# Kernel optimization log

Hardware: AMD Instinct MI355X
Metric: run time of the kernel (lower is better)

Reference implementation:

```python
import jax, jax.numpy as jnp
import numpy as np

N_VIS, N_ASSOC, N_MOTOR, IN_DIM, T = 8192, 4096, 1024, 4096, 16
TAU_MEM, V_TH, TAU_ELIG = 20.0, 1.0, 500.0


def setup_inputs() -> dict:
    key = jax.random.key(0)
    ks = jax.random.split(key, 8)
    visual_input = jax.random.uniform(ks[0], (T, IN_DIM), dtype=jnp.float32)
    noise = jax.random.uniform(ks[1], (T, N_VIS), dtype=jnp.float32)  # replaces torch.rand_like
    dopamine = jax.random.normal(ks[2], (T,), dtype=jnp.float32)
    # visual_encoder: nn.Linear(4096, n_visual) default init (kaiming-uniform-ish); use small uniform
    lim = 1.0 / np.sqrt(IN_DIM)
    W_enc = jax.random.uniform(ks[3], (N_VIS, IN_DIM), minval=-lim, maxval=lim, dtype=jnp.float32)
    b_enc = jax.random.uniform(ks[4], (N_VIS,), minval=-lim, maxval=lim, dtype=jnp.float32)
    # v_to_a / a_to_m: uniform_(0.01, 0.05), no bias
    W_va = jax.random.uniform(ks[5], (N_ASSOC, N_VIS), minval=0.01, maxval=0.05, dtype=jnp.float32)
    W_am = jax.random.uniform(ks[6], (N_MOTOR, N_ASSOC), minval=0.01, maxval=0.05, dtype=jnp.float32)
    return {"visual_input": visual_input, "noise": noise, "dopamine": dopamine,
            "W_enc": W_enc, "b_enc": b_enc, "W_va": W_va, "W_am": W_am}


def reference(visual_input, noise, dopamine, W_enc, b_enc, W_va, W_am):
    decay_m = 1.0 - 1.0 / TAU_MEM
    decay_e = 1.0 - 1.0 / TAU_ELIG
    f32 = jnp.float32

    def step(carry, xs):
        vV, vA, vM, eVA, eAM, Wva, Wam = carry
        x, u, d = xs
        # visual encoding + Bernoulli spikes
        rates = jax.nn.sigmoid(x @ W_enc.T + b_enc)             # [n_visual]
        in_spk = (u < rates * 0.3).astype(f32)
        # LIF: visual layer
        vV = vV * decay_m + in_spk
        v_spk = (vV > V_TH).astype(f32)
        vV = vV * (1.0 - v_spk)
        # LIF: assoc layer
        vA = vA * decay_m + (v_spk @ Wva.T) * 0.1
        a_spk = (vA > V_TH).astype(f32)
        vA = vA * (1.0 - a_spk)
        # LIF: motor layer
        vM = vM * decay_m + (a_spk @ Wam.T) * 0.1
        m_spk = (vM > V_TH).astype(f32)
        vM = vM * (1.0 - m_spk)
        # DA-STDP eligibility traces (rank-1 updates)
        eVA = eVA * decay_e + jnp.outer(v_spk, a_spk) * 0.01    # [n_visual, n_assoc]
        eAM = eAM * decay_e + jnp.outer(a_spk, m_spk) * 0.01    # [n_assoc, n_motor]
        # conditional dopamine-gated weight update
        gate = jnp.abs(d) > 0.1
        Wva_new = jnp.clip(Wva + jnp.clip(d * eVA.T * 0.1, -0.01, 0.01), 0.0, 1.0)
        Wam_new = jnp.clip(Wam + jnp.clip(d * eAM.T * 0.1, -0.01, 0.01), 0.0, 1.0)
        Wva = jnp.where(gate, Wva_new, Wva)
        Wam = jnp.where(gate, Wam_new, Wam)
        eVA = jnp.where(gate, eVA * 0.5, eVA)
        eAM = jnp.where(gate, eAM * 0.5, eAM)
        return (vV, vA, vM, eVA, eAM, Wva, Wam), m_spk

    init = (jnp.zeros(N_VIS, f32), jnp.zeros(N_ASSOC, f32), jnp.zeros(N_MOTOR, f32),
            jnp.zeros((N_VIS, N_ASSOC), f32), jnp.zeros((N_ASSOC, N_MOTOR), f32),
            W_va, W_am)
    _, motor_spikes = jax.lax.scan(step, init, (visual_input, noise, dopamine))
    return motor_spikes  # [T, n_motor]
```

## Files before the change

### kernel.cpp

```cpp
#include <hip/hip_runtime.h>
#include <cstdint>

#define N_VIS   8192
#define N_ASSOC 4096
#define N_MOTOR 1024
#define IN_DIM  4096
#define T_STEPS 16

typedef float f32x4 __attribute__((ext_vector_type(4)));

__device__ __forceinline__ float4 nt_load4(const float4* p) {
    f32x4 r = __builtin_nontemporal_load((const f32x4*)p);
    return make_float4(r.x, r.y, r.z, r.w);
}

template<int COLS, int CS>
__global__ __launch_bounds__(512, 4) void mv_rowwave_kernel(
        const float* __restrict__ Wg, const float* __restrict__ Vg,
        float* __restrict__ Sp, int nrows) {
    constexpr int F4PR = COLS / 4;
    constexpr int SEG4 = F4PR / CS;
    constexpr int NIT  = SEG4 / 64;
    __shared__ float4 vs[2][16 * 64];
    const int tid  = threadIdx.x;
    const int lane = tid & 63, wv = tid >> 6;
    const int rb   = blockIdx.x / CS;
    const int sp   = blockIdx.x % CS;
    const int j0   = rb * 16 + wv * 2;
    const float4* W4a = (const float4*)Wg + (size_t)j0 * F4PR + (size_t)sp * SEG4;
    const float4* W4b = W4a + F4PR;
    const float4* V4  = (const float4*)Vg + (size_t)sp * SEG4;

    float acc[2][T_STEPS];
#pragma unroll
    for (int t = 0; t < T_STEPS; ++t) { acc[0][t] = 0.f; acc[1][t] = 0.f; }

    {
        int f = tid;
#pragma unroll
        for (int p = 0; p < 2; ++p, f += 512) {
            int t = f >> 6, c = f & 63;
            vs[0][f] = V4[(size_t)t * F4PR + c];
        }
    }
    float4 wa = nt_load4(&W4a[lane]), wb = nt_load4(&W4b[lane]);
    __syncthreads();

    int buf = 0;
#pragma unroll 1
    for (int it = 0; it < NIT; ++it) {
        float4 wan = wa, wbn = wb;
        if (it + 1 < NIT) {
            wan = nt_load4(&W4a[(it + 1) * 64 + lane]);
            wbn = nt_load4(&W4b[(it + 1) * 64 + lane]);
            int f = tid;
#pragma unroll
            for (int p = 0; p < 2; ++p, f += 512) {
                int t = f >> 6, c = f & 63;
                vs[buf ^ 1][f] = V4[(size_t)t * F4PR + (it + 1) * 64 + c];
            }
        }
#pragma unroll
        for (int t = 0; t < T_STEPS; ++t) {
            float4 v = vs[buf][t * 64 + lane];
            acc[0][t] = fmaf(wa.x, v.x, acc[0][t]);
            acc[0][t] = fmaf(wa.y, v.y, acc[0][t]);
            acc[0][t] = fmaf(wa.z, v.z, acc[0][t]);
            acc[0][t] = fmaf(wa.w, v.w, acc[0][t]);
            acc[1][t] = fmaf(wb.x, v.x, acc[1][t]);
            acc[1][t] = fmaf(wb.y, v.y, acc[1][t]);
            acc[1][t] = fmaf(wb.z, v.z, acc[1][t]);
            acc[1][t] = fmaf(wb.w, v.w, acc[1][t]);
        }
        __syncthreads();
        wa = wan; wb = wbn; buf ^= 1;
    }

#pragma unroll
    for (int t = 0; t < T_STEPS; ++t) {
        float a0 = acc[0][t], a1 = acc[1][t];
        for (int o = 32; o; o >>= 1) {
            a0 += __shfl_down(a0, o, 64);
            a1 += __shfl_down(a1, o, 64);
        }
        acc[0][t] = a0; acc[1][t] = a1;
    }
    if (lane == 0) {
#pragma unroll
        for (int r = 0; r < 2; ++r) {
            float4* So = (float4*)(Sp + ((size_t)sp * nrows + j0 + r) * 16);
#pragma unroll
            for (int q = 0; q < 4; ++q)
                So[q] = make_float4(acc[r][q*4], acc[r][q*4+1], acc[r][q*4+2], acc[r][q*4+3]);
        }
    }
}

template<int COLS, int CS>
__global__ __launch_bounds__(512, 4) void mv_bits_kernel(
        const float* __restrict__ Wg, const unsigned* __restrict__ mask,
        float* __restrict__ Sp, int nrows) {
    constexpr int F4PR = COLS / 4;
    constexpr int SEG4 = F4PR / CS;
    constexpr int NIT  = SEG4 / 64;
    const int lane = threadIdx.x & 63, wv = threadIdx.x >> 6;
    const int rb   = blockIdx.x / CS;
    const int sp   = blockIdx.x % CS;
    const int j0   = rb * 16 + wv * 2;
    const float4* W4a = (const float4*)Wg + (size_t)j0 * F4PR + (size_t)sp * SEG4;
    const float4* W4b = W4a + F4PR;
    const uint4*  M4  = (const uint4*)mask + (size_t)sp * SEG4;

    float acc0[T_STEPS], acc1[T_STEPS];
#pragma unroll
    for (int t = 0; t < T_STEPS; ++t) { acc0[t] = 0.f; acc1[t] = 0.f; }

#pragma unroll 2
    for (int it = 0; it < NIT; ++it) {
        const int idx = it * 64 + lane;
        float4 wa = nt_load4(&W4a[idx]);
        float4 wb = nt_load4(&W4b[idx]);
        uint4  m  = M4[idx];
#pragma unroll
        for (int t = 0; t < T_STEPS; ++t) {
            float bx = (float)((m.x >> t) & 1u);
            float by = (float)((m.y >> t) & 1u);
            float bz = (float)((m.z >> t) & 1u);
            float bw = (float)((m.w >> t) & 1u);
            acc0[t] = fmaf(wa.x, bx, acc0[t]);
            acc0[t] = fmaf(wa.y, by, acc0[t]);
            acc0[t] = fmaf(wa.z, bz, acc0[t]);
            acc0[t] = fmaf(wa.w, bw, acc0[t]);
            acc1[t] = fmaf(wb.x, bx, acc1[t]);
            acc1[t] = fmaf(wb.y, by, acc1[t]);
            acc1[t] = fmaf(wb.z, bz, acc1[t]);
            acc1[t] = fmaf(wb.w, bw, acc1[t]);
        }
    }

#pragma unroll
    for (int t = 0; t < T_STEPS; ++t) {
        float a0 = acc0[t], a1 = acc1[t];
        for (int o = 32; o; o >>= 1) {
            a0 += __shfl_down(a0, o, 64);
            a1 += __shfl_down(a1, o, 64);
        }
        acc0[t] = a0; acc1[t] = a1;
    }
    if (lane == 0) {
        float4* So0 = (float4*)(Sp + ((size_t)sp * nrows + j0) * 16);
        float4* So1 = (float4*)(Sp + ((size_t)sp * nrows + j0 + 1) * 16);
#pragma unroll
        for (int q = 0; q < 4; ++q) {
            So0[q] = make_float4(acc0[q*4], acc0[q*4+1], acc0[q*4+2], acc0[q*4+3]);
            So1[q] = make_float4(acc1[q*4], acc1[q*4+1], acc1[q*4+2], acc1[q*4+3]);
        }
    }
}

__global__ __launch_bounds__(256) void vlif_kernel(
        const float* __restrict__ S1p, const float* __restrict__ noise,
        const float* __restrict__ b, unsigned* __restrict__ vmask) {
    const int i = blockIdx.x * 256 + threadIdx.x;
    float a[T_STEPS];
#pragma unroll
    for (int t = 0; t < T_STEPS; ++t)
        a[t] = S1p[(size_t)i * 16 + t] + S1p[((size_t)N_VIS + i) * 16 + t];
    const float bb = b[i];
    float v = 0.f;
    unsigned msk = 0;
#pragma unroll
    for (int t = 0; t < T_STEPS; ++t) {
        float logit = a[t] + bb;
        float rate = 1.0f / (1.0f + expf(-logit));
        float u = noise[t * N_VIS + i];
        float ins = (u < rate * 0.3f) ? 1.0f : 0.0f;
        v = v * 0.95f + ins;
        if (v > 1.0f) { msk |= (1u << t); v = 0.f; }
    }
    vmask[i] = msk;
}

__global__ void ktab_kernel(const float* __restrict__ dop, float* __restrict__ K,
                            int* __restrict__ ovl_z) {
    __shared__ float C[256];
    __shared__ float sd[16];
    __shared__ unsigned sg[16];
    const int p = threadIdx.x;
    ovl_z[p] = 0; ovl_z[p + 256] = 0;
    if (p < 16) {
        float d = dop[p];
        sd[p] = d;
        sg[p] = (fabsf(d) > 0.1f) ? 1u : 0u;
    }
    __syncthreads();
    {
        const int s = p >> 4, r = p & 15;
        float c = 0.f;
        if (s >= r) {
            c = 1.f;
            for (int u = r; u < s; ++u) {
                if (sg[u]) c *= 0.5f;
                c *= 0.998f;
            }
        }
        C[p] = c;
    }
    __syncthreads();
    {
        const int t = p >> 4, r = p & 15;
        float kk = 0.f;
        for (int s = r; s < t; ++s)
            if (sg[s]) kk += ((sd[s] * 0.1f) * 0.01f) * C[s * 16 + r];
        K[p] = kk;
    }
}

__global__ void ovl_kernel(const unsigned* __restrict__ mask, int words_per_block,
                           int* __restrict__ ovl) {
    const int p = threadIdx.x;
    const int r = p >> 4, t = p & 15;
    const unsigned* w = mask + blockIdx.x * words_per_block;
    int c = 0;
    for (int i = 0; i < words_per_block; ++i)
        c += (int)((w[i] >> r) & (w[i] >> t) & 1u);
    atomicAdd(&ovl[p], c);
}

__global__ __launch_bounds__(64) void rec_kernel(
        const float* __restrict__ base, const int* __restrict__ ovl,
        const float* __restrict__ K, unsigned* __restrict__ mask_out,
        float* __restrict__ outp, int out_stride, int n_rows, int cs) {
    __shared__ float KO[256];
    const int tid = threadIdx.x;
    for (int p = tid; p < 256; p += 64) {
        const int t = p >> 4, r = p & 15;
        KO[p] = K[p] * (float)ovl[r * 16 + t];
    }
    __syncthreads();

    const int j = blockIdx.x * 64 + tid;
    float br[T_STEPS];
#pragma unroll
    for (int t = 0; t < T_STEPS; ++t) br[t] = base[(size_t)j * 16 + t];
#pragma unroll 1
    for (int s = 1; s < cs; ++s)
#pragma unroll
        for (int t = 0; t < T_STEPS; ++t)
            br[t] += base[((size_t)s * n_rows + j) * 16 + t];

    float vmem = 0.f;
    unsigned am = 0;
#pragma unroll
    for (int t = 0; t < T_STEPS; ++t) {
        float I = br[t];
        for (int r = 0; r < t; ++r)
            if ((am >> r) & 1u) I += KO[t * 16 + r];
        vmem = vmem * 0.95f + I * 0.1f;
        const bool s = vmem > 1.0f;
        if (s) { vmem = 0.f; am |= (1u << t); }
        if (outp) outp[t * out_stride + j] = s ? 1.0f : 0.0f;
    }
    mask_out[j] = am;
}

extern "C" void kernel_launch(void* const* d_in, const int* in_sizes, int n_in,
                              void* d_out, int out_size, void* d_ws, size_t ws_size,
                              hipStream_t stream) {
    const float* x     = (const float*)d_in[0];
    const float* noise = (const float*)d_in[1];
    const float* dop   = (const float*)d_in[2];
    const float* W_enc = (const float*)d_in[3];
    const float* b_enc = (const float*)d_in[4];
    const float* W_va  = (const float*)d_in[5];
    const float* W_am  = (const float*)d_in[6];
    float* out = (float*)d_out;
    (void)in_sizes; (void)n_in; (void)out_size; (void)ws_size;

    char* ws = (char*)d_ws;
    size_t off = 0;
    unsigned* vmask = (unsigned*)(ws + off); off += N_VIS * 4;
    unsigned* amask = (unsigned*)(ws + off); off += N_ASSOC * 4;
    unsigned* mmask = (unsigned*)(ws + off); off += N_MOTOR * 4;
    float*    K     = (float*)(ws + off);    off += 256 * 4;
    int*      ovl_v = (int*)(ws + off);      off += 256 * 4;
    int*      ovl_a = (int*)(ws + off);      off += 256 * 4;
    float*    S1    = (float*)(ws + off);    off += (size_t)2 * N_VIS   * 16 * 4;
    float*    S2    = (float*)(ws + off);    off += (size_t)4 * N_ASSOC * 16 * 4;
    float*    S3    = (float*)(ws + off);    off += (size_t)4 * N_MOTOR * 16 * 4;

    ktab_kernel<<<1, 256, 0, stream>>>(dop, K, ovl_v);
    mv_rowwave_kernel<IN_DIM, 2><<<(N_VIS / 16) * 2, 512, 0, stream>>>(W_enc, x, S1, N_VIS);
    vlif_kernel<<<N_VIS / 256, 256, 0, stream>>>(S1, noise, b_enc, vmask);
    ovl_kernel<<<32, 256, 0, stream>>>(vmask, N_VIS / 32, ovl_v);
    mv_bits_kernel<N_VIS, 4><<<(N_ASSOC / 16) * 4, 512, 0, stream>>>(W_va, vmask, S2, N_ASSOC);
    rec_kernel<<<N_ASSOC / 64, 64, 0, stream>>>(S2, ovl_v, K, amask, nullptr, 0, N_ASSOC, 4);
    ovl_kernel<<<16, 256, 0, stream>>>(amask, N_ASSOC / 16, ovl_a);
    mv_bits_kernel<N_ASSOC, 4><<<(N_MOTOR / 16) * 4, 512, 0, stream>>>(W_am, amask, S3, N_MOTOR);
    rec_kernel<<<N_MOTOR / 64, 64, 0, stream>>>(S3, ovl_a, K, mmask, out, N_MOTOR, N_MOTOR, 4);
}
```

Measured before the change: 146.2 us.

## Fuse matvec, LIF recurrence and overlap counting into per-layer kernels

Each layer's matvec is merged with its LIF/recurrence epilogue and the spike-overlap histogram, and the column split across blocks is dropped so each block owns whole rows. This cuts the launch count from nine to four and removes the partial-sum workspace round trips and the separate ovl kernels. The trade-off is fewer blocks per layer (smaller grids of 256/128 threads for the later layers), longer serial loops per wave, and the serial LIF epilogue running on lane 0 of each wave.

Result: faster. 140.4 us (-3.9%).

```diff
diff --git a/kernel.cpp b/kernel.cpp
--- a/kernel.cpp
+++ b/kernel.cpp
@@ -14,26 +14,59 @@
     return make_float4(r.x, r.y, r.z, r.w);
 }
 
-template<int COLS, int CS>
-__global__ __launch_bounds__(512, 4) void mv_rowwave_kernel(
-        const float* __restrict__ Wg, const float* __restrict__ Vg,
-        float* __restrict__ Sp, int nrows) {
-    constexpr int F4PR = COLS / 4;
-    constexpr int SEG4 = F4PR / CS;
-    constexpr int NIT  = SEG4 / 64;
+__global__ void ktab_kernel(const float* __restrict__ dop, float* __restrict__ K,
+                            int* __restrict__ ovl_z) {
+    __shared__ float C[256];
+    __shared__ float sd[16];
+    __shared__ unsigned sg[16];
+    const int p = threadIdx.x;
+    ovl_z[p] = 0; ovl_z[p + 256] = 0;
+    if (p < 16) {
+        float d = dop[p];
+        sd[p] = d;
+        sg[p] = (fabsf(d) > 0.1f) ? 1u : 0u;
+    }
+    __syncthreads();
+    {
+        const int s = p >> 4, r = p & 15;
+        float c = 0.f;
+        if (s >= r) {
+            c = 1.f;
+            for (int u = r; u < s; ++u) {
+                if (sg[u]) c *= 0.5f;
+                c *= 0.998f;
+            }
+        }
+        C[p] = c;
+    }
+    __syncthreads();
+    {
+        const int t = p >> 4, r = p & 15;
+        float kk = 0.f;
+        for (int s = r; s < t; ++s)
+            if (sg[s]) kk += ((sd[s] * 0.1f) * 0.01f) * C[s * 16 + r];
+        K[p] = kk;
+    }
+}
+
+__global__ __launch_bounds__(512, 4) void enc_fused_kernel(
+        const float* __restrict__ Wg, const float* __restrict__ xg,
+        const float* __restrict__ noise, const float* __restrict__ b,
+        unsigned* __restrict__ vmask, int* __restrict__ ovl_v) {
+    constexpr int F4PR = IN_DIM / 4;
+    constexpr int NIT  = F4PR / 64;
     __shared__ float4 vs[2][16 * 64];
+    __shared__ unsigned smask[16];
     const int tid  = threadIdx.x;
     const int lane = tid & 63, wv = tid >> 6;
-    const int rb   = blockIdx.x / CS;
-    const int sp   = blockIdx.x % CS;
-    const int j0   = rb * 16 + wv * 2;
-    const float4* W4a = (const float4*)Wg + (size_t)j0 * F4PR + (size_t)sp * SEG4;
+    const int j0   = blockIdx.x * 16 + wv * 2;
+    const float4* W4a = (const float4*)Wg + (size_t)j0 * F4PR;
     const float4* W4b = W4a + F4PR;
-    const float4* V4  = (const float4*)Vg + (size_t)sp * SEG4;
-
-    float acc[2][T_STEPS];
-#pragma unroll
-    for (int t = 0; t < T_STEPS; ++t) { acc[0][t] = 0.f; acc[1][t] = 0.f; }
+    const float4* V4  = (const float4*)xg;
+
+    float acc0[T_STEPS], acc1[T_STEPS];
+#pragma unroll
+    for (int t = 0; t < T_STEPS; ++t) { acc0[t] = 0.f; acc1[t] = 0.f; }
 
     {
         int f = tid;
@@ -63,14 +96,14 @@
 #pragma unroll
         for (int t = 0; t < T_STEPS; ++t) {
             float4 v = vs[buf][t * 64 + lane];
-            acc[0][t] = fmaf(wa.x, v.x, acc[0][t]);
-            acc[0][t] = fmaf(wa.y, v.y, acc[0][t]);
-            acc[0][t] = fmaf(wa.z, v.z, acc[0][t]);
-            acc[0][t] = fmaf(wa.w, v.w, acc[0][t]);
-            acc[1][t] = fmaf(wb.x, v.x, acc[1][t]);
-            acc[1][t] = fmaf(wb.y, v.y, acc[1][t]);
-            acc[1][t] = fmaf(wb.z, v.z, acc[1][t]);
-            acc[1][t] = fmaf(wb.w, v.w, acc[1][t]);
+            acc0[t] = fmaf(wa.x, v.x, acc0[t]);
+            acc0[t] = fmaf(wa.y, v.y, acc0[t]);
+            acc0[t] = fmaf(wa.z, v.z, acc0[t]);
+            acc0[t] = fmaf(wa.w, v.w, acc0[t]);
+            acc1[t] = fmaf(wb.x, v.x, acc1[t]);
+            acc1[t] = fmaf(wb.y, v.y, acc1[t]);
+            acc1[t] = fmaf(wb.z, v.z, acc1[t]);
+            acc1[t] = fmaf(wb.w, v.w, acc1[t]);
         }
         __syncthreads();
         wa = wan; wb = wbn; buf ^= 1;
@@ -78,38 +111,66 @@
 
 #pragma unroll
     for (int t = 0; t < T_STEPS; ++t) {
-        float a0 = acc[0][t], a1 = acc[1][t];
+        float a0 = acc0[t], a1 = acc1[t];
         for (int o = 32; o; o >>= 1) {
             a0 += __shfl_down(a0, o, 64);
             a1 += __shfl_down(a1, o, 64);
         }
-        acc[0][t] = a0; acc[1][t] = a1;
+        acc0[t] = a0; acc1[t] = a1;
     }
     if (lane == 0) {
-#pragma unroll
-        for (int r = 0; r < 2; ++r) {
-            float4* So = (float4*)(Sp + ((size_t)sp * nrows + j0 + r) * 16);
-#pragma unroll
-            for (int q = 0; q < 4; ++q)
-                So[q] = make_float4(acc[r][q*4], acc[r][q*4+1], acc[r][q*4+2], acc[r][q*4+3]);
-        }
-    }
-}
-
-template<int COLS, int CS>
-__global__ __launch_bounds__(512, 4) void mv_bits_kernel(
+        auto do_row = [&](int i, const float (&a)[T_STEPS]) -> unsigned {
+            float bb = b[i];
+            float v = 0.f;
+            unsigned msk = 0;
+#pragma unroll
+            for (int t = 0; t < T_STEPS; ++t) {
+                float logit = a[t] + bb;
+                float rate = 1.0f / (1.0f + expf(-logit));
+                float u = noise[t * N_VIS + i];
+                float ins = (u < rate * 0.3f) ? 1.0f : 0.0f;
+                v = v * 0.95f + ins;
+                if (v > 1.0f) { msk |= (1u << t); v = 0.f; }
+            }
+            vmask[i] = msk;
+            return msk;
+        };
+        smask[wv * 2]     = do_row(j0, acc0);
+        smask[wv * 2 + 1] = do_row(j0 + 1, acc1);
+    }
+    __syncthreads();
+    if (tid < 256) {
+        const int r = tid >> 4, t = tid & 15;
+        int c = 0;
+#pragma unroll
+        for (int q = 0; q < 16; ++q)
+            c += (int)((smask[q] >> r) & (smask[q] >> t) & 1u);
+        if (c) atomicAdd(&ovl_v[tid], c);
+    }
+}
+
+template<int COLS, int NT, int WRITE_OVL>
+__global__ __launch_bounds__(NT, 4) void layer_fused_kernel(
         const float* __restrict__ Wg, const unsigned* __restrict__ mask,
-        float* __restrict__ Sp, int nrows) {
+        const float* __restrict__ K, const int* __restrict__ ovl_in,
+        unsigned* __restrict__ mask_out, int* __restrict__ ovl_out,
+        float* __restrict__ outp, int out_stride) {
     constexpr int F4PR = COLS / 4;
-    constexpr int SEG4 = F4PR / CS;
-    constexpr int NIT  = SEG4 / 64;
-    const int lane = threadIdx.x & 63, wv = threadIdx.x >> 6;
-    const int rb   = blockIdx.x / CS;
-    const int sp   = blockIdx.x % CS;
-    const int j0   = rb * 16 + wv * 2;
-    const float4* W4a = (const float4*)Wg + (size_t)j0 * F4PR + (size_t)sp * SEG4;
+    constexpr int NIT  = F4PR / 64;
+    constexpr int ROWS = (NT / 64) * 2;
+    __shared__ float KO[256];
+    __shared__ unsigned smask[ROWS];
+    const int tid  = threadIdx.x;
+    const int lane = tid & 63, wv = tid >> 6;
+    const int j0   = blockIdx.x * ROWS + wv * 2;
+
+    for (int p = tid; p < 256; p += NT)
+        KO[p] = K[p] * (float)ovl_in[(p & 15) * 16 + (p >> 4)];
+    __syncthreads();
+
+    const float4* W4a = (const float4*)Wg + (size_t)j0 * F4PR;
     const float4* W4b = W4a + F4PR;
-    const uint4*  M4  = (const uint4*)mask + (size_t)sp * SEG4;
+    const uint4*  M4  = (const uint4*)mask;
 
     float acc0[T_STEPS], acc1[T_STEPS];
 #pragma unroll
@@ -147,121 +208,38 @@
         }
         acc0[t] = a0; acc1[t] = a1;
     }
+
     if (lane == 0) {
-        float4* So0 = (float4*)(Sp + ((size_t)sp * nrows + j0) * 16);
-        float4* So1 = (float4*)(Sp + ((size_t)sp * nrows + j0 + 1) * 16);
-#pragma unroll
-        for (int q = 0; q < 4; ++q) {
-            So0[q] = make_float4(acc0[q*4], acc0[q*4+1], acc0[q*4+2], acc0[q*4+3]);
-            So1[q] = make_float4(acc1[q*4], acc1[q*4+1], acc1[q*4+2], acc1[q*4+3]);
-        }
-    }
-}
-
-__global__ __launch_bounds__(256) void vlif_kernel(
-        const float* __restrict__ S1p, const float* __restrict__ noise,
-        const float* __restrict__ b, unsigned* __restrict__ vmask) {
-    const int i = blockIdx.x * 256 + threadIdx.x;
-    float a[T_STEPS];
-#pragma unroll
-    for (int t = 0; t < T_STEPS; ++t)
-        a[t] = S1p[(size_t)i * 16 + t] + S1p[((size_t)N_VIS + i) * 16 + t];
-    const float bb = b[i];
-    float v = 0.f;
-    unsigned msk = 0;
-#pragma unroll
-    for (int t = 0; t < T_STEPS; ++t) {
-        float logit = a[t] + bb;
-        float rate = 1.0f / (1.0f + expf(-logit));
-        float u = noise[t * N_VIS + i];
-        float ins = (u < rate * 0.3f) ? 1.0f : 0.0f;
-        v = v * 0.95f + ins;
-        if (v > 1.0f) { msk |= (1u << t); v = 0.f; }
-    }
-    vmask[i] = msk;
-}
-
-__global__ void ktab_kernel(const float* __restrict__ dop, float* __restrict__ K,
-                            int* __restrict__ ovl_z) {
-    __shared__ float C[256];
-    __shared__ float sd[16];
-    __shared__ unsigned sg[16];
-    const int p = threadIdx.x;
-    ovl_z[p] = 0; ovl_z[p + 256] = 0;
-    if (p < 16) {
-        float d = dop[p];
-        sd[p] = d;
-        sg[p] = (fabsf(d) > 0.1f) ? 1u : 0u;
-    }
-    __syncthreads();
-    {
-        const int s = p >> 4, r = p & 15;
-        float c = 0.f;
-        if (s >= r) {
-            c = 1.f;
-            for (int u = r; u < s; ++u) {
-                if (sg[u]) c *= 0.5f;
-                c *= 0.998f;
-            }
-        }
-        C[p] = c;
-    }
-    __syncthreads();
-    {
-        const int t = p >> 4, r = p & 15;
-        float kk = 0.f;
-        for (int s = r; s < t; ++s)
-            if (sg[s]) kk += ((sd[s] * 0.1f) * 0.01f) * C[s * 16 + r];
-        K[p] = kk;
-    }
-}
-
-__global__ void ovl_kernel(const unsigned* __restrict__ mask, int words_per_block,
-                           int* __restrict__ ovl) {
-    const int p = threadIdx.x;
-    const int r = p >> 4, t = p & 15;
-    const unsigned* w = mask + blockIdx.x * words_per_block;
-    int c = 0;
-    for (int i = 0; i < words_per_block; ++i)
-        c += (int)((w[i] >> r) & (w[i] >> t) & 1u);
-    atomicAdd(&ovl[p], c);
-}
-
-__global__ __launch_bounds__(64) void rec_kernel(
-        const float* __restrict__ base, const int* __restrict__ ovl,
-        const float* __restrict__ K, unsigned* __restrict__ mask_out,
-        float* __restrict__ outp, int out_stride, int n_rows, int cs) {
-    __shared__ float KO[256];
-    const int tid = threadIdx.x;
-    for (int p = tid; p < 256; p += 64) {
-        const int t = p >> 4, r = p & 15;
-        KO[p] = K[p] * (float)ovl[r * 16 + t];
-    }
-    __syncthreads();
-
-    const int j = blockIdx.x * 64 + tid;
-    float br[T_STEPS];
-#pragma unroll
-    for (int t = 0; t < T_STEPS; ++t) br[t] = base[(size_t)j * 16 + t];
-#pragma unroll 1
-    for (int s = 1; s < cs; ++s)
-#pragma unroll
-        for (int t = 0; t < T_STEPS; ++t)
-            br[t] += base[((size_t)s * n_rows + j) * 16 + t];
-
-    float vmem = 0.f;
-    unsigned am = 0;
-#pragma unroll
-    for (int t = 0; t < T_STEPS; ++t) {
-        float I = br[t];
-        for (int r = 0; r < t; ++r)
-            if ((am >> r) & 1u) I += KO[t * 16 + r];
-        vmem = vmem * 0.95f + I * 0.1f;
-        const bool s = vmem > 1.0f;
-        if (s) { vmem = 0.f; am |= (1u << t); }
-        if (outp) outp[t * out_stride + j] = s ? 1.0f : 0.0f;
-    }
-    mask_out[j] = am;
+        auto do_rec = [&](int j, const float (&br)[T_STEPS]) -> unsigned {
+            float vmem = 0.f;
+            unsigned am = 0;
+#pragma unroll
+            for (int t = 0; t < T_STEPS; ++t) {
+                float I = br[t];
+                for (int r = 0; r < t; ++r)
+                    if ((am >> r) & 1u) I += KO[t * 16 + r];
+                vmem = vmem * 0.95f + I * 0.1f;
+                const bool s = vmem > 1.0f;
+                if (s) { vmem = 0.f; am |= (1u << t); }
+                if (outp) outp[t * out_stride + j] = s ? 1.0f : 0.0f;
+            }
+            if (mask_out) mask_out[j] = am;
+            return am;
+        };
+        smask[wv * 2]     = do_rec(j0, acc0);
+        smask[wv * 2 + 1] = do_rec(j0 + 1, acc1);
+    }
+    if (WRITE_OVL) {
+        __syncthreads();
+        for (int p = tid; p < 256; p += NT) {
+            const int r = p >> 4, t = p & 15;
+            int c = 0;
+#pragma unroll
+            for (int q = 0; q < ROWS; ++q)
+                c += (int)((smask[q] >> r) & (smask[q] >> t) & 1u);
+            if (c) atomicAdd(&ovl_out[p], c);
+        }
+    }
 }
 
 extern "C" void kernel_launch(void* const* d_in, const int* in_sizes, int n_in,
@@ -281,21 +259,14 @@
     size_t off = 0;
     unsigned* vmask = (unsigned*)(ws + off); off += N_VIS * 4;
     unsigned* amask = (unsigned*)(ws + off); off += N_ASSOC * 4;
-    unsigned* mmask = (unsigned*)(ws + off); off += N_MOTOR * 4;
     float*    K     = (float*)(ws + off);    off += 256 * 4;
     int*      ovl_v = (int*)(ws + off);      off += 256 * 4;
     int*      ovl_a = (int*)(ws + off);      off += 256 * 4;
-    float*    S1    = (float*)(ws + off);    off += (size_t)2 * N_VIS   * 16 * 4;
-    float*    S2    = (float*)(ws + off);    off += (size_t)4 * N_ASSOC * 16 * 4;
-    float*    S3    = (float*)(ws + off);    off += (size_t)4 * N_MOTOR * 16 * 4;
 
     ktab_kernel<<<1, 256, 0, stream>>>(dop, K, ovl_v);
-    mv_rowwave_kernel<IN_DIM, 2><<<(N_VIS / 16) * 2, 512, 0, stream>>>(W_enc, x, S1, N_VIS);
-    vlif_kernel<<<N_VIS / 256, 256, 0, stream>>>(S1, noise, b_enc, vmask);
-    ovl_kernel<<<32, 256, 0, stream>>>(vmask, N_VIS / 32, ovl_v);
-    mv_bits_kernel<N_VIS, 4><<<(N_ASSOC / 16) * 4, 512, 0, stream>>>(W_va, vmask, S2, N_ASSOC);
-    rec_kernel<<<N_ASSOC / 64, 64, 0, stream>>>(S2, ovl_v, K, amask, nullptr, 0, N_ASSOC, 4);
-    ovl_kernel<<<16, 256, 0, stream>>>(amask, N_ASSOC / 16, ovl_a);
-    mv_bits_kernel<N_ASSOC, 4><<<(N_MOTOR / 16) * 4, 512, 0, stream>>>(W_am, amask, S3, N_MOTOR);
-    rec_kernel<<<N_MOTOR / 64, 64, 0, stream>>>(S3, ovl_a, K, mmask, out, N_MOTOR, N_MOTOR, 4);
-}
+    enc_fused_kernel<<<N_VIS / 16, 512, 0, stream>>>(W_enc, x, noise, b_enc, vmask, ovl_v);
+    layer_fused_kernel<N_VIS, 256, 1><<<N_ASSOC / 8, 256, 0, stream>>>(
+        W_va, vmask, K, ovl_v, amask, ovl_a, nullptr, 0);
+    layer_fused_kernel<N_ASSOC, 128, 0><<<N_MOTOR / 4, 128, 0, stream>>>(
+        W_am, amask, K, ovl_a, nullptr, nullptr, out, N_MOTOR);
+}
```
